# Performance work log

Hardware: AMD Instinct MI355X
Metric: run time of the kernel (lower is better)

Reference implementation:

```python
import jax, jax.numpy as jnp
import numpy as np

N_HEADS = 8
CHUNK = 512


def _mha(x, Wq, Wk, Wv, Wo, n_heads):
    # Standard no-bias multi-head self-attention; torch Linear => x @ W.T
    B, T, d = x.shape
    hd = d // n_heads
    q = (x @ Wq.T).reshape(B, T, n_heads, hd)
    k = (x @ Wk.T).reshape(B, T, n_heads, hd)
    v = (x @ Wv.T).reshape(B, T, n_heads, hd)
    scores = jnp.einsum('bqhd,bkhd->bhqk', q, k) / jnp.sqrt(jnp.asarray(hd, x.dtype))
    attn = jax.nn.softmax(scores, axis=-1)
    out = jnp.einsum('bhqk,bkhd->bqhd', attn, v).reshape(B, T, d)
    return out @ Wo.T


def _cross_chunk_attn(s, n_heads):
    # SDPA over chunk summaries with q=k=v=s (no projections inside)
    B, nc, d = s.shape
    hd = d // n_heads
    q = s.reshape(B, nc, n_heads, hd)
    scores = jnp.einsum('bqhd,bkhd->bhqk', q, q) / jnp.sqrt(jnp.asarray(hd, s.dtype))
    attn = jax.nn.softmax(scores, axis=-1)
    out = jnp.einsum('bhqk,bkhd->bqhd', attn, q).reshape(B, nc, d)
    return out


def setup_inputs() -> dict:
    key = jax.random.key(0)
    ks = jax.random.split(key, 6)
    B, T, d = 2, 16384, 512
    scale = 1.0 / np.sqrt(d)
    x = jax.random.normal(ks[0], (B, T, d), dtype=jnp.float32)
    Wq = jax.random.normal(ks[1], (d, d), dtype=jnp.float32) * scale
    Wk = jax.random.normal(ks[2], (d, d), dtype=jnp.float32) * scale
    Wv = jax.random.normal(ks[3], (d, d), dtype=jnp.float32) * scale
    Wo = jax.random.normal(ks[4], (d, d), dtype=jnp.float32) * scale
    Wg = jax.random.normal(ks[5], (d, d), dtype=jnp.float32) * scale
    return {'x': x, 'Wq': Wq, 'Wk': Wk, 'Wv': Wv, 'Wo': Wo, 'Wg': Wg}


def reference(x, Wq, Wk, Wv, Wo, Wg):
    B, T, d = x.shape
    pad = (CHUNK - T % CHUNK) % CHUNK
    if pad > 0:
        x = jnp.pad(x, ((0, 0), (0, pad), (0, 0)))
    T_padded = T + pad
    n_chunks = T_padded // CHUNK
    # 1) chunk: (B*n_chunks, CHUNK, d)
    chunked = x.reshape(B * n_chunks, CHUNK, d)
    # 2) local attention within each chunk
    local_out = _mha(chunked, Wq, Wk, Wv, Wo, N_HEADS)
    # 3) mean-pool summaries -> (B, n_chunks, d)
    summaries = local_out.mean(axis=1).reshape(B, n_chunks, d)
    # 4) global projection + cross-chunk SDPA
    global_ctx = _cross_chunk_attn(summaries @ Wg.T, N_HEADS)
    # 5) broadcast chunk context back to tokens
    enriched = local_out + global_ctx.reshape(B * n_chunks, 1, d)
    # 6) recombine and trim padding
    out = enriched.reshape(B, T_padded, d)
    if pad > 0:
        out = out[:, :T, :]
    return out
```

## Files before the change

### kernel.cpp

```cpp
#include <hip/hip_runtime.h>

typedef __attribute__((ext_vector_type(8))) short short8;
typedef __attribute__((ext_vector_type(4))) float f32x4;
typedef __attribute__((ext_vector_type(16))) float f32x16;

#define DEV static __device__ __forceinline__

DEV float bf2f(unsigned short u) {
  union { unsigned int u32; float f; } v; v.u32 = ((unsigned int)u) << 16; return v.f;
}
DEV unsigned short f2bf(float f) {
  union { float f; unsigned int u; } v; v.f = f;
  unsigned int r = v.u + 0x7fffu + ((v.u >> 16) & 1u);
  return (unsigned short)(r >> 16);
}
DEV unsigned cvtpk(float lo, float hi) {
  unsigned r;
  asm("v_cvt_pk_bf16_f32 %0, %1, %2" : "=v"(r) : "v"(lo), "v"(hi));
  return r;
}
DEV void plswap(unsigned &a, unsigned &b) {
  asm("v_permlane32_swap_b32 %0, %1" : "+v"(a), "+v"(b));
}
DEV short8 mk8(unsigned a, unsigned b, unsigned c, unsigned d) {
  union { unsigned u[4]; short8 v; } x;
  x.u[0] = a; x.u[1] = b; x.u[2] = c; x.u[3] = d; return x.v;
}
DEV float fexp2(float x) {
  float r;
  asm("v_exp_f32 %0, %1" : "=v"(r) : "v"(x));
  return r;
}

#define GLL16(g, l) __builtin_amdgcn_global_load_lds( \
    (const __attribute__((address_space(1))) void*)(g), \
    (__attribute__((address_space(3))) void*)(l), 16, 0, 0)

constexpr int D  = 512;
constexpr int BT = 32768;

__global__ __launch_bounds__(256) void k_convert(
    const float* __restrict__ x, const float* __restrict__ Wq, const float* __restrict__ Wk,
    const float* __restrict__ Wv, const float* __restrict__ Wo,
    unsigned short* __restrict__ xb, unsigned short* __restrict__ wqkv,
    unsigned short* __restrict__ wo_b) {
  int idx = blockIdx.x * 256 + threadIdx.x;
  const int NX4 = (BT * D) / 4;
  const float* src; unsigned short* dst; size_t i4;
  if (idx < NX4) {
    src = x; dst = xb; i4 = (size_t)idx * 4;
  } else {
    int t = idx - NX4;
    int w = t >> 16;
    int within = t & 65535;
    src = (w == 0) ? Wq : (w == 1) ? Wk : (w == 2) ? Wv : Wo;
    dst = (w < 3) ? (wqkv + (size_t)w * D * D) : wo_b;
    i4 = (size_t)within * 4;
  }
  float4 v = *(const float4*)(src + i4);
  ushort4 o; o.x = f2bf(v.x); o.y = f2bf(v.y); o.z = f2bf(v.z); o.w = f2bf(v.w);
  *(ushort4*)(dst + i4) = o;
}

template<int NBLK, int EPI>
__global__ __launch_bounds__(512, 4) void k_gemm(
    const unsigned short* __restrict__ A, const unsigned short* __restrict__ Bm,
    unsigned short* __restrict__ O0, unsigned short* __restrict__ O1,
    unsigned short* __restrict__ O2) {
  __shared__ unsigned short Ash[3][128 * 32];
  __shared__ unsigned short Bsh[3][256 * 32];
  const int tid = threadIdx.x;
  const int lane = tid & 63, w = tid >> 6;
  const int lr = lane & 15, lg = lane >> 4;
  const int cpx = gridDim.x >> 3;
  const int bid = blockIdx.x;
  const int work = (bid & 7) * cpx + (bid >> 3);
  const int nb = work % NBLK, mb = work / NBLK;
  const int m0 = mb * 128, n0 = nb * 256;
  const int wr = w >> 2, wc = w & 3;

  const int sr = lane >> 2;
  const int sg8 = ((lane & 3) ^ ((lane >> 3) & 3)) * 8;
  const unsigned short* gA  = A  + (size_t)(m0 + w * 16 + sr) * D + sg8;
  const unsigned short* gB0 = Bm + (size_t)(n0 + w * 16 + sr) * D + sg8;
  const unsigned short* gB1 = Bm + (size_t)(n0 + 128 + w * 16 + sr) * D + sg8;

  auto stage = [&](int kt, int b) {
    GLL16(gA  + kt * 32, &Ash[b][w * 512]);
    GLL16(gB0 + kt * 32, &Bsh[b][w * 512]);
    GLL16(gB1 + kt * 32, &Bsh[b][(128 + w * 16) * 32]);
  };

  f32x4 acc[4][4];
  #pragma unroll
  for (int m = 0; m < 4; ++m)
    #pragma unroll
    for (int n = 0; n < 4; ++n) acc[m][n] = (f32x4){0.f, 0.f, 0.f, 0.f};

  stage(0, 0);
  stage(1, 1);

  const int rdsw = (lg ^ ((lr >> 1) & 3)) * 8;

#define GSTEP(KT, WN) { \
    asm volatile("s_waitcnt vmcnt(" #WN ")" ::: "memory"); \
    __builtin_amdgcn_s_barrier(); \
    if ((KT) + 2 < 16) stage((KT) + 2, ((KT) + 2) % 3); \
    const unsigned short* Ac = Ash[(KT) % 3]; \
    const unsigned short* Bc = Bsh[(KT) % 3]; \
    short8 af[4], bf[4]; \
    _Pragma("unroll") \
    for (int m = 0; m < 4; ++m) \
      af[m] = *(const short8*)&Ac[(wr * 64 + m * 16 + lr) * 32 + rdsw]; \
    _Pragma("unroll") \
    for (int n = 0; n < 4; ++n) \
      bf[n] = *(const short8*)&Bc[(wc * 64 + n * 16 + lr) * 32 + rdsw]; \
    __builtin_amdgcn_s_setprio(1); \
    _Pragma("unroll") \
    for (int m = 0; m < 4; ++m) \
      _Pragma("unroll") \
      for (int n = 0; n < 4; ++n) \
        acc[m][n] = __builtin_amdgcn_mfma_f32_16x16x32_bf16(af[m], bf[n], acc[m][n], 0, 0, 0); \
    __builtin_amdgcn_s_setprio(0); \
  }

  GSTEP(0, 3)  GSTEP(1, 3)  GSTEP(2, 3)  GSTEP(3, 3)
  GSTEP(4, 3)  GSTEP(5, 3)  GSTEP(6, 3)  GSTEP(7, 3)
  GSTEP(8, 3)  GSTEP(9, 3)  GSTEP(10, 3) GSTEP(11, 3)
  GSTEP(12, 3) GSTEP(13, 3) GSTEP(14, 3) GSTEP(15, 0)
#undef GSTEP

  if (EPI == 1 && nb >= 4) {
    #pragma unroll
    for (int m = 0; m < 4; ++m) {
      #pragma unroll
      for (int n = 0; n < 4; ++n) {
        int e = (n0 - 1024) + wc * 64 + n * 16 + lr;
        int grow = m0 + wr * 64 + m * 16 + lg * 4;
        int bc = grow >> 9, key = grow & 511;
        ushort4 pk;
        pk.x = f2bf(acc[m][n][0]); pk.y = f2bf(acc[m][n][1]);
        pk.z = f2bf(acc[m][n][2]); pk.w = f2bf(acc[m][n][3]);
        *(ushort4*)&O2[(size_t)(bc * 512 + e) * 512 + key] = pk;
      }
    }
  } else {
    unsigned short* Od = O0;
    int cshift = 0;
    float cs = (EPI == 1 && nb < 2) ? 0.1803368801f : 1.0f;
    if (EPI == 1 && nb >= 2) { Od = O1; cshift = 512; }
    #pragma unroll
    for (int m = 0; m < 4; ++m) {
      #pragma unroll
      for (int n = 0; n < 4; ++n) {
        int col = n0 + wc * 64 + n * 16 + lr - cshift;
        #pragma unroll
        for (int r = 0; r < 4; ++r) {
          int row = m0 + wr * 64 + m * 16 + lg * 4 + r;
          Od[(size_t)row * D + col] = f2bf(acc[m][n][r] * cs);
        }
      }
    }
  }
}

__global__ __launch_bounds__(512, 4) void k_attn(
    const unsigned short* __restrict__ Q, const unsigned short* __restrict__ K,
    const unsigned short* __restrict__ Vt, unsigned short* __restrict__ attn_out) {
  __shared__ char lds[3][16384];
  const int tid = threadIdx.x;
  const int lane = tid & 63, w = tid >> 6;
  const int l31 = lane & 31, hl = lane >> 5;
  int work = ((blockIdx.x & 7) << 7) + (blockIdx.x >> 3);
  int qh = work & 1, h = (work >> 1) & 7, bc = work >> 4;
  int qbase = bc * 512 + qh * 256 + w * 32;

  short8 qf[4];
  {
    const unsigned short* qp = Q + (size_t)(qbase + l31) * D + h * 64 + hl * 8;
    #pragma unroll
    for (int ks = 0; ks < 4; ++ks) qf[ks] = *(const short8*)(qp + ks * 16);
  }

  const int lr3 = lane >> 3;
  const int srow = w * 8 + lr3;
  const int sq = (lane & 7) ^ ((lr3 + w) & 7);
  const unsigned short* gK = K  + (size_t)(bc * 512 + srow) * D + h * 64 + sq * 8;
  const unsigned short* gV = Vt + (size_t)(bc * 512 + h * 64 + srow) * D + sq * 8;
  auto STAGE = [&](int T, int B) {
    GLL16(gK + (size_t)(T) * 64 * D, &lds[B][w * 1024]);
    GLL16(gV + (T) * 64,             &lds[B][8192 + w * 1024]);
  };

  f32x16 oA, oB;
  #pragma unroll
  for (int i = 0; i < 16; ++i) { oA[i] = 0.f; oB[i] = 0.f; }
  float mrun = -3e38f, lrun = 0.f;
  const int f0 = (l31 + (l31 >> 3)) & 7;
  const int f1 = (f0 + 4) & 7;

  STAGE(0, 0);
  STAGE(1, 1);

  #pragma unroll
  for (int t = 0; t < 8; ++t) {
    if (t == 0 || t == 7) asm volatile("s_waitcnt vmcnt(0)" ::: "memory");
    else                  asm volatile("s_waitcnt vmcnt(2)" ::: "memory");
    __builtin_amdgcn_s_barrier();
    if (t < 6) STAGE(t + 2, (t + 2) % 3);
    const char* kb = lds[t % 3];
    const char* vb = lds[t % 3] + 8192;

    f32x16 sA, sB;
    #pragma unroll
    for (int i = 0; i < 16; ++i) { sA[i] = 0.f; sB[i] = 0.f; }
    #pragma unroll
    for (int ks = 0; ks < 4; ++ks) {
      int c = ks * 2 + hl;
      short8 kf0 = *(const short8*)(kb + l31 * 128 + ((c ^ f0) << 4));
      short8 kf1 = *(const short8*)(kb + (32 + l31) * 128 + ((c ^ f1) << 4));
      sA = __builtin_amdgcn_mfma_f32_32x32x16_bf16(kf0, qf[ks], sA, 0, 0, 0);
      sB = __builtin_amdgcn_mfma_f32_32x32x16_bf16(kf1, qf[ks], sB, 0, 0, 0);
    }

    float pm = fmaxf(sA[0], sA[1]);
    #pragma unroll
    for (int i = 2; i < 16; i += 2) pm = fmaxf(pm, fmaxf(sA[i], sA[i + 1]));
    #pragma unroll
    for (int i = 0; i < 16; i += 2) pm = fmaxf(pm, fmaxf(sB[i], sB[i + 1]));
    pm = fmaxf(pm, __shfl_xor(pm, 32));
    if (!__all(pm - mrun <= 8.f)) {
      float mnew = fmaxf(mrun, pm);
      float alpha = fexp2(mrun - mnew);
      mrun = mnew;
      lrun *= alpha;
      #pragma unroll
      for (int i = 0; i < 16; ++i) { oA[i] *= alpha; oB[i] *= alpha; }
    }
    float ls = 0.f;
    #pragma unroll
    for (int i = 0; i < 16; ++i) { float p = fexp2(sA[i] - mrun); sA[i] = p; ls += p; }
    #pragma unroll
    for (int i = 0; i < 16; ++i) { float p = fexp2(sB[i] - mrun); sB[i] = p; ls += p; }
    ls += __shfl_xor(ls, 32);
    lrun += ls;

    unsigned dA[8], dB[8];
    #pragma unroll
    for (int i = 0; i < 8; ++i) {
      dA[i] = cvtpk(sA[2 * i], sA[2 * i + 1]);
      dB[i] = cvtpk(sB[2 * i], sB[2 * i + 1]);
    }
    plswap(dA[0], dA[2]); plswap(dA[1], dA[3]);
    plswap(dA[4], dA[6]); plswap(dA[5], dA[7]);
    plswap(dB[0], dB[2]); plswap(dB[1], dB[3]);
    plswap(dB[4], dB[6]); plswap(dB[5], dB[7]);
    short8 pf[4] = { mk8(dA[0], dA[1], dA[2], dA[3]), mk8(dA[4], dA[5], dA[6], dA[7]),
                     mk8(dB[0], dB[1], dB[2], dB[3]), mk8(dB[4], dB[5], dB[6], dB[7]) };

    #pragma unroll
    for (int k4 = 0; k4 < 4; ++k4) {
      int c = k4 * 2 + hl;
      short8 vf0 = *(const short8*)(vb + l31 * 128 + ((c ^ f0) << 4));
      short8 vf1 = *(const short8*)(vb + (32 + l31) * 128 + ((c ^ f1) << 4));
      oA = __builtin_amdgcn_mfma_f32_32x32x16_bf16(vf0, pf[k4], oA, 0, 0, 0);
      oB = __builtin_amdgcn_mfma_f32_32x32x16_bf16(vf1, pf[k4], oB, 0, 0, 0);
    }
  }

  __syncthreads();
  float inv = 1.f / lrun;
  const int x7 = l31 & 7;
  char* tr = &lds[0][0] + w * 4096;
  #pragma unroll
  for (int r = 0; r < 16; ++r) {
    int e0 = (r & 3) + 8 * (r >> 2) + 4 * hl;
    *(unsigned short*)(tr + ((l31 * 128 + e0 * 2) ^ (x7 << 4)))        = f2bf(oA[r] * inv);
    *(unsigned short*)(tr + ((l31 * 128 + (32 + e0) * 2) ^ (x7 << 4))) = f2bf(oB[r] * inv);
  }
  unsigned short* op = attn_out + (size_t)(qbase + l31) * D + h * 64 + hl * 32;
  #pragma unroll
  for (int s = 0; s < 4; ++s) {
    int slot = (hl * 4 + s) ^ x7;
    short8 v = *(const short8*)(tr + l31 * 128 + slot * 16);
    *(short8*)(op + s * 8) = v;
  }
}

__global__ __launch_bounds__(256) void k_mean(const unsigned short* __restrict__ lout,
                                              float* __restrict__ summ) {
  int bc = blockIdx.x;
  int col = blockIdx.y * 256 + threadIdx.x;
  const unsigned short* p = lout + (size_t)bc * 512 * 512 + col;
  float s = 0.f;
  #pragma unroll 8
  for (int r = 0; r < 512; ++r) s += bf2f(p[(size_t)r * 512]);
  summ[bc * 512 + col] = s * (1.f / 512.f);
}

__global__ __launch_bounds__(256) void k_sg(const float* __restrict__ summ,
                                            const float* __restrict__ Wg,
                                            float* __restrict__ sg) {
  __shared__ float srow[512];
  int m = blockIdx.x >> 1, half = blockIdx.x & 1;
  for (int i = threadIdx.x; i < 512; i += 256) srow[i] = summ[m * 512 + i];
  __syncthreads();
  int n = half * 256 + threadIdx.x;
  const float* wr = Wg + (size_t)n * 512;
  float s = 0.f;
  #pragma unroll 8
  for (int kk = 0; kk < 512; ++kk) s += srow[kk] * wr[kk];
  sg[m * 512 + n] = s;
}

__global__ __launch_bounds__(256) void k_gattn(const float* __restrict__ sg,
                                               float* __restrict__ gctx) {
  __shared__ float qs[32][64];
  __shared__ float sc[32][32];
  int b = blockIdx.x >> 3, h = blockIdx.x & 7;
  int tid = threadIdx.x;
  for (int i = tid; i < 2048; i += 256) {
    int r = i >> 6, e = i & 63;
    qs[r][e] = sg[(size_t)(b * 32 + r) * 512 + h * 64 + e];
  }
  __syncthreads();
  for (int p = tid; p < 1024; p += 256) {
    int qi = p >> 5, ki = p & 31;
    float s = 0.f;
    #pragma unroll 8
    for (int e = 0; e < 64; ++e) s += qs[qi][e] * qs[ki][e];
    sc[qi][ki] = s * 0.125f;
  }
  __syncthreads();
  if (tid < 32) {
    float mx = -1e30f;
    for (int k2 = 0; k2 < 32; ++k2) mx = fmaxf(mx, sc[tid][k2]);
    float sm = 0.f;
    for (int k2 = 0; k2 < 32; ++k2) { float p = __expf(sc[tid][k2] - mx); sc[tid][k2] = p; sm += p; }
    float iv = 1.f / sm;
    for (int k2 = 0; k2 < 32; ++k2) sc[tid][k2] *= iv;
  }
  __syncthreads();
  for (int i = tid; i < 2048; i += 256) {
    int r = i >> 6, e = i & 63;
    float o = 0.f;
    #pragma unroll 8
    for (int k2 = 0; k2 < 32; ++k2) o += sc[r][k2] * qs[k2][e];
    gctx[(size_t)(b * 32 + r) * 512 + h * 64 + e] = o;
  }
}

__global__ __launch_bounds__(256) void k_final(const unsigned short* __restrict__ lout,
                                               const float* __restrict__ gctx,
                                               float* __restrict__ out) {
  size_t idx = (size_t)blockIdx.x * 256 + threadIdx.x;
  size_t i = idx * 8;
  int c = (int)(i & 511);
  int bcg = (int)(i >> 18);
  const float* g = gctx + (size_t)bcg * 512 + c;
  ushort4 lv0 = *(const ushort4*)(lout + i);
  ushort4 lv1 = *(const ushort4*)(lout + i + 4);
  float4 g0 = *(const float4*)(g);
  float4 g1 = *(const float4*)(g + 4);
  float4 o0, o1;
  o0.x = bf2f(lv0.x) + g0.x; o0.y = bf2f(lv0.y) + g0.y;
  o0.z = bf2f(lv0.z) + g0.z; o0.w = bf2f(lv0.w) + g0.w;
  o1.x = bf2f(lv1.x) + g1.x; o1.y = bf2f(lv1.y) + g1.y;
  o1.z = bf2f(lv1.z) + g1.z; o1.w = bf2f(lv1.w) + g1.w;
  *(float4*)(out + i) = o0;
  *(float4*)(out + i + 4) = o1;
}

extern "C" void kernel_launch(void* const* d_in, const int* in_sizes, int n_in,
                              void* d_out, int out_size, void* d_ws, size_t ws_size,
                              hipStream_t stream) {
  const float* x  = (const float*)d_in[0];
  const float* Wq = (const float*)d_in[1];
  const float* Wk = (const float*)d_in[2];
  const float* Wv = (const float*)d_in[3];
  const float* Wo = (const float*)d_in[4];
  const float* Wg = (const float*)d_in[5];
  float* out = (float*)d_out;

  char* ws = (char*)d_ws;
  unsigned short* xb   = (unsigned short*)(ws);
  unsigned short* q    = (unsigned short*)(ws + 33554432);
  unsigned short* kb   = (unsigned short*)(ws + 67108864);
  unsigned short* vt   = (unsigned short*)(ws + 100663296);
  unsigned short* wqkv = (unsigned short*)(ws + 134217728);
  unsigned short* wo_b = (unsigned short*)(ws + 135790592);
  float* summ = (float*)(ws + 136314880);
  float* sgp  = (float*)(ws + 136445952);
  float* gctx = (float*)(ws + 136577024);
  unsigned short* attn_out = xb;
  unsigned short* local_bf = q;

  k_convert<<<17408, 256, 0, stream>>>(x, Wq, Wk, Wv, Wo, xb, wqkv, wo_b);
  k_gemm<6, 1><<<1536, 512, 0, stream>>>(xb, wqkv, q, kb, vt);
  k_attn<<<1024, 512, 0, stream>>>(q, kb, vt, attn_out);
  k_gemm<2, 0><<<512, 512, 0, stream>>>(attn_out, wo_b, local_bf, nullptr, nullptr);
  k_mean<<<dim3(64, 2), 256, 0, stream>>>(local_bf, summ);
  k_sg<<<128, 256, 0, stream>>>(summ, Wg, sgp);
  k_gattn<<<16, 256, 0, stream>>>(sgp, gctx);
  k_final<<<8192, 256, 0, stream>>>(local_bf, gctx, out);
}
```

Measured before the change: 235.3 us.

## Process both query halves per attention block to share K/V tiles

Each k_attn block now handles all 512 queries of a (chunk, head) pair instead of 256. Every wave keeps two query fragment sets, accumulators and softmax states, and runs both halves against each staged K/V tile. The grid shrinks from 1024 to 512 blocks. The goal is to halve global-to-LDS K/V traffic and staging overhead, at the cost of roughly doubled register pressure (possible spills under the 512-thread launch bound) and fewer blocks to fill the CUs.

New measurement: 277.7 us. 1.18x slower.

```diff
diff --git a/kernel.cpp b/kernel.cpp
--- a/kernel.cpp
+++ b/kernel.cpp
@@ -171,15 +171,19 @@
   const int tid = threadIdx.x;
   const int lane = tid & 63, w = tid >> 6;
   const int l31 = lane & 31, hl = lane >> 5;
-  int work = ((blockIdx.x & 7) << 7) + (blockIdx.x >> 3);
-  int qh = work & 1, h = (work >> 1) & 7, bc = work >> 4;
-  int qbase = bc * 512 + qh * 256 + w * 32;
-
-  short8 qf[4];
+  int work = ((blockIdx.x & 7) << 6) + (blockIdx.x >> 3);
+  int h = work & 7, bc = work >> 3;
+  int qbase = bc * 512 + w * 32;
+
+  short8 qf0[4], qf1[4];
   {
-    const unsigned short* qp = Q + (size_t)(qbase + l31) * D + h * 64 + hl * 8;
-    #pragma unroll
-    for (int ks = 0; ks < 4; ++ks) qf[ks] = *(const short8*)(qp + ks * 16);
+    const unsigned short* qp0 = Q + (size_t)(qbase + l31) * D + h * 64 + hl * 8;
+    const unsigned short* qp1 = qp0 + (size_t)256 * D;
+    #pragma unroll
+    for (int ks = 0; ks < 4; ++ks) {
+      qf0[ks] = *(const short8*)(qp0 + ks * 16);
+      qf1[ks] = *(const short8*)(qp1 + ks * 16);
+    }
   }
 
   const int lr3 = lane >> 3;
@@ -192,15 +196,70 @@
     GLL16(gV + (T) * 64,             &lds[B][8192 + w * 1024]);
   };
 
-  f32x16 oA, oB;
+  f32x16 oA0, oB0, oA1, oB1;
   #pragma unroll
-  for (int i = 0; i < 16; ++i) { oA[i] = 0.f; oB[i] = 0.f; }
-  float mrun = -3e38f, lrun = 0.f;
+  for (int i = 0; i < 16; ++i) { oA0[i] = 0.f; oB0[i] = 0.f; oA1[i] = 0.f; oB1[i] = 0.f; }
+  float mrun0 = -3e38f, lrun0 = 0.f, mrun1 = -3e38f, lrun1 = 0.f;
   const int f0 = (l31 + (l31 >> 3)) & 7;
   const int f1 = (f0 + 4) & 7;
 
   STAGE(0, 0);
   STAGE(1, 1);
+
+#define PROC_HALF(QF, OA, OB, MRUN, LRUN) { \
+    f32x16 sA, sB; \
+    _Pragma("unroll") \
+    for (int i = 0; i < 16; ++i) { sA[i] = 0.f; sB[i] = 0.f; } \
+    _Pragma("unroll") \
+    for (int ks = 0; ks < 4; ++ks) { \
+      int c = ks * 2 + hl; \
+      short8 kf0 = *(const short8*)(kb + l31 * 128 + ((c ^ f0) << 4)); \
+      short8 kf1 = *(const short8*)(kb + (32 + l31) * 128 + ((c ^ f1) << 4)); \
+      sA = __builtin_amdgcn_mfma_f32_32x32x16_bf16(kf0, QF[ks], sA, 0, 0, 0); \
+      sB = __builtin_amdgcn_mfma_f32_32x32x16_bf16(kf1, QF[ks], sB, 0, 0, 0); \
+    } \
+    float pm = fmaxf(sA[0], sA[1]); \
+    _Pragma("unroll") \
+    for (int i = 2; i < 16; i += 2) pm = fmaxf(pm, fmaxf(sA[i], sA[i + 1])); \
+    _Pragma("unroll") \
+    for (int i = 0; i < 16; i += 2) pm = fmaxf(pm, fmaxf(sB[i], sB[i + 1])); \
+    pm = fmaxf(pm, __shfl_xor(pm, 32)); \
+    if (!__all(pm - MRUN <= 8.f)) { \
+      float mnew = fmaxf(MRUN, pm); \
+      float alpha = fexp2(MRUN - mnew); \
+      MRUN = mnew; \
+      LRUN *= alpha; \
+      _Pragma("unroll") \
+      for (int i = 0; i < 16; ++i) { OA[i] *= alpha; OB[i] *= alpha; } \
+    } \
+    float ls = 0.f; \
+    _Pragma("unroll") \
+    for (int i = 0; i < 16; ++i) { float p = fexp2(sA[i] - MRUN); sA[i] = p; ls += p; } \
+    _Pragma("unroll") \
+    for (int i = 0; i < 16; ++i) { float p = fexp2(sB[i] - MRUN); sB[i] = p; ls += p; } \
+    ls += __shfl_xor(ls, 32); \
+    LRUN += ls; \
+    unsigned dA[8], dB[8]; \
+    _Pragma("unroll") \
+    for (int i = 0; i < 8; ++i) { \
+      dA[i] = cvtpk(sA[2 * i], sA[2 * i + 1]); \
+      dB[i] = cvtpk(sB[2 * i], sB[2 * i + 1]); \
+    } \
+    plswap(dA[0], dA[2]); plswap(dA[1], dA[3]); \
+    plswap(dA[4], dA[6]); plswap(dA[5], dA[7]); \
+    plswap(dB[0], dB[2]); plswap(dB[1], dB[3]); \
+    plswap(dB[4], dB[6]); plswap(dB[5], dB[7]); \
+    short8 pf[4] = { mk8(dA[0], dA[1], dA[2], dA[3]), mk8(dA[4], dA[5], dA[6], dA[7]), \
+                     mk8(dB[0], dB[1], dB[2], dB[3]), mk8(dB[4], dB[5], dB[6], dB[7]) }; \
+    _Pragma("unroll") \
+    for (int k4 = 0; k4 < 4; ++k4) { \
+      int c = k4 * 2 + hl; \
+      short8 vf0 = *(const short8*)(vb + l31 * 128 + ((c ^ f0) << 4)); \
+      short8 vf1 = *(const short8*)(vb + (32 + l31) * 128 + ((c ^ f1) << 4)); \
+      OA = __builtin_amdgcn_mfma_f32_32x32x16_bf16(vf0, pf[k4], OA, 0, 0, 0); \
+      OB = __builtin_amdgcn_mfma_f32_32x32x16_bf16(vf1, pf[k4], OB, 0, 0, 0); \
+    } \
+  }
 
   #pragma unroll
   for (int t = 0; t < 8; ++t) {
@@ -210,80 +269,45 @@
     if (t < 6) STAGE(t + 2, (t + 2) % 3);
     const char* kb = lds[t % 3];
     const char* vb = lds[t % 3] + 8192;
-
-    f32x16 sA, sB;
-    #pragma unroll
-    for (int i = 0; i < 16; ++i) { sA[i] = 0.f; sB[i] = 0.f; }
-    #pragma unroll
-    for (int ks = 0; ks < 4; ++ks) {
-      int c = ks * 2 + hl;
-      short8 kf0 = *(const short8*)(kb + l31 * 128 + ((c ^ f0) << 4));
-      short8 kf1 = *(const short8*)(kb + (32 + l31) * 128 + ((c ^ f1) << 4));
-      sA = __builtin_amdgcn_mfma_f32_32x32x16_bf16(kf0, qf[ks], sA, 0, 0, 0);
-      sB = __builtin_amdgcn_mfma_f32_32x32x16_bf16(kf1, qf[ks], sB, 0, 0, 0);
-    }
-
-    float pm = fmaxf(sA[0], sA[1]);
-    #pragma unroll
-    for (int i = 2; i < 16; i += 2) pm = fmaxf(pm, fmaxf(sA[i], sA[i + 1]));
-    #pragma unroll
-    for (int i = 0; i < 16; i += 2) pm = fmaxf(pm, fmaxf(sB[i], sB[i + 1]));
-    pm = fmaxf(pm, __shfl_xor(pm, 32));
-    if (!__all(pm - mrun <= 8.f)) {
-      float mnew = fmaxf(mrun, pm);
-      float alpha = fexp2(mrun - mnew);
-      mrun = mnew;
-      lrun *= alpha;
-      #pragma unroll
-      for (int i = 0; i < 16; ++i) { oA[i] *= alpha; oB[i] *= alpha; }
-    }
-    float ls = 0.f;
-    #pragma unroll
-    for (int i = 0; i < 16; ++i) { float p = fexp2(sA[i] - mrun); sA[i] = p; ls += p; }
-    #pragma unroll
-    for (int i = 0; i < 16; ++i) { float p = fexp2(sB[i] - mrun); sB[i] = p; ls += p; }
-    ls += __shfl_xor(ls, 32);
-    lrun += ls;
-
-    unsigned dA[8], dB[8];
-    #pragma unroll
-    for (int i = 0; i < 8; ++i) {
-      dA[i] = cvtpk(sA[2 * i], sA[2 * i + 1]);
-      dB[i] = cvtpk(sB[2 * i], sB[2 * i + 1]);
-    }
-    plswap(dA[0], dA[2]); plswap(dA[1], dA[3]);
-    plswap(dA[4], dA[6]); plswap(dA[5], dA[7]);
-    plswap(dB[0], dB[2]); plswap(dB[1], dB[3]);
-    plswap(dB[4], dB[6]); plswap(dB[5], dB[7]);
-    short8 pf[4] = { mk8(dA[0], dA[1], dA[2], dA[3]), mk8(dA[4], dA[5], dA[6], dA[7]),
-                     mk8(dB[0], dB[1], dB[2], dB[3]), mk8(dB[4], dB[5], dB[6], dB[7]) };
-
-    #pragma unroll
-    for (int k4 = 0; k4 < 4; ++k4) {
-      int c = k4 * 2 + hl;
-      short8 vf0 = *(const short8*)(vb + l31 * 128 + ((c ^ f0) << 4));
-      short8 vf1 = *(const short8*)(vb + (32 + l31) * 128 + ((c ^ f1) << 4));
-      oA = __builtin_amdgcn_mfma_f32_32x32x16_bf16(vf0, pf[k4], oA, 0, 0, 0);
-      oB = __builtin_amdgcn_mfma_f32_32x32x16_bf16(vf1, pf[k4], oB, 0, 0, 0);
-    }
-  }
+    PROC_HALF(qf0, oA0, oB0, mrun0, lrun0)
+    PROC_HALF(qf1, oA1, oB1, mrun1, lrun1)
+  }
+#undef PROC_HALF
 
   __syncthreads();
-  float inv = 1.f / lrun;
   const int x7 = l31 & 7;
   char* tr = &lds[0][0] + w * 4096;
-  #pragma unroll
-  for (int r = 0; r < 16; ++r) {
-    int e0 = (r & 3) + 8 * (r >> 2) + 4 * hl;
-    *(unsigned short*)(tr + ((l31 * 128 + e0 * 2) ^ (x7 << 4)))        = f2bf(oA[r] * inv);
-    *(unsigned short*)(tr + ((l31 * 128 + (32 + e0) * 2) ^ (x7 << 4))) = f2bf(oB[r] * inv);
-  }
-  unsigned short* op = attn_out + (size_t)(qbase + l31) * D + h * 64 + hl * 32;
-  #pragma unroll
-  for (int s = 0; s < 4; ++s) {
-    int slot = (hl * 4 + s) ^ x7;
-    short8 v = *(const short8*)(tr + l31 * 128 + slot * 16);
-    *(short8*)(op + s * 8) = v;
+  {
+    float inv = 1.f / lrun0;
+    #pragma unroll
+    for (int r = 0; r < 16; ++r) {
+      int e0 = (r & 3) + 8 * (r >> 2) + 4 * hl;
+      *(unsigned short*)(tr + ((l31 * 128 + e0 * 2) ^ (x7 << 4)))        = f2bf(oA0[r] * inv);
+      *(unsigned short*)(tr + ((l31 * 128 + (32 + e0) * 2) ^ (x7 << 4))) = f2bf(oB0[r] * inv);
+    }
+    unsigned short* op = attn_out + (size_t)(qbase + l31) * D + h * 64 + hl * 32;
+    #pragma unroll
+    for (int s = 0; s < 4; ++s) {
+      int slot = (hl * 4 + s) ^ x7;
+      short8 v = *(const short8*)(tr + l31 * 128 + slot * 16);
+      *(short8*)(op + s * 8) = v;
+    }
+  }
+  {
+    float inv = 1.f / lrun1;
+    #pragma unroll
+    for (int r = 0; r < 16; ++r) {
+      int e0 = (r & 3) + 8 * (r >> 2) + 4 * hl;
+      *(unsigned short*)(tr + ((l31 * 128 + e0 * 2) ^ (x7 << 4)))        = f2bf(oA1[r] * inv);
+      *(unsigned short*)(tr + ((l31 * 128 + (32 + e0) * 2) ^ (x7 << 4))) = f2bf(oB1[r] * inv);
+    }
+    unsigned short* op = attn_out + (size_t)(qbase + 256 + l31) * D + h * 64 + hl * 32;
+    #pragma unroll
+    for (int s = 0; s < 4; ++s) {
+      int slot = (hl * 4 + s) ^ x7;
+      short8 v = *(const short8*)(tr + l31 * 128 + slot * 16);
+      *(short8*)(op + s * 8) = v;
+    }
   }
 }
 
@@ -397,7 +421,7 @@
 
   k_convert<<<17408, 256, 0, stream>>>(x, Wq, Wk, Wv, Wo, xb, wqkv, wo_b);
   k_gemm<6, 1><<<1536, 512, 0, stream>>>(xb, wqkv, q, kb, vt);
-  k_attn<<<1024, 512, 0, stream>>>(q, kb, vt, attn_out);
+  k_attn<<<512, 512, 0, stream>>>(q, kb, vt, attn_out);
   k_gemm<2, 0><<<512, 512, 0, stream>>>(attn_out, wo_b, local_bf, nullptr, nullptr);
   k_mean<<<dim3(64, 2), 256, 0, stream>>>(local_bf, summ);
   k_sg<<<128, 256, 0, stream>>>(summ, Wg, sgp);
```
